# Kernel tuning notes

Measured on AMD Instinct MI355X. Metric: run time of the kernel, lower is better.

The kernel has to match this reference:

```python
import jax, jax.numpy as jnp
import numpy as np

FP8_MAX = 448.0  # max finite value of float8_e4m3fn


def _fp8_quant(v, scale):
    # emulate saturating scaled cast to float8_e4m3fn, then dequant-free fp8 storage (upcast to f32 for the gemm)
    q = jnp.clip(v / scale, -FP8_MAX, FP8_MAX)
    return q.astype(jnp.float8_e4m3fn).astype(jnp.float32)


def setup_inputs() -> dict:
    key = jax.random.key(0)
    k0, k1, k2, k3 = jax.random.split(key, 4)
    T, H, I, E = 1024, 1024, 2816, 8
    x = jax.random.normal(k0, (T, H), jnp.float32)
    router_logits = jax.random.normal(k1, (T, E), jnp.float32)
    w13_weight = jax.random.normal(k2, (E, 2 * I, H), jnp.float32) * 0.02
    w2_weight = jax.random.normal(k3, (E, H, I), jnp.float32) * 0.02
    return {
        "x": x,
        "router_logits": router_logits,
        "w13_weight": w13_weight,
        "w2_weight": w2_weight,
        "w13_input_scale": jnp.ones((E,), jnp.float32),
        "w2_input_scale": jnp.ones((E,), jnp.float32),
        "top_k": 2,
    }


def reference(x, router_logits, w13_weight, w2_weight, w13_input_scale, w2_input_scale, top_k):
    T, H = x.shape
    E, two_I, _ = w13_weight.shape
    I = two_I // 2

    # --- routing: softmax -> top_k -> renormalize (select_experts) ---
    probs = jax.nn.softmax(router_logits, axis=-1)
    topk_w, topk_ids = jax.lax.top_k(probs, top_k)            # [T,K]
    topk_w = topk_w / jnp.sum(topk_w, axis=-1, keepdims=True)
    # dense combine matrix [T,E]: sparsity of the grouped gemm dispatch
    combine = jnp.zeros((T, E), x.dtype).at[jnp.arange(T)[:, None], topk_ids].add(topk_w)

    # --- per-expert fp8 weight quantization (ops.scaled_fp8_quant per expert) ---
    w13_scale = jnp.max(jnp.abs(w13_weight), axis=(1, 2)) / FP8_MAX  # [E]
    w2_scale = jnp.max(jnp.abs(w2_weight), axis=(1, 2)) / FP8_MAX
    w13_q = _fp8_quant(w13_weight, w13_scale[:, None, None])         # [E,2I,H]
    w2_q = _fp8_quant(w2_weight, w2_scale[:, None, None])            # [E,H,I]

    # --- grouped gemm 1: per-expert activation quant + fp8 gemm + dequant scale ---
    x_q = _fp8_quant(x[None], w13_input_scale[:, None, None])        # [E,T,H]
    h = jnp.einsum('eth,eih->eti', x_q, w13_q) * (w13_input_scale * w13_scale)[:, None, None]

    # --- silu_and_mul: gate = first intermediate_size rows, up = second ---
    act = jax.nn.silu(h[..., :I]) * h[..., I:]                       # [E,T,I]

    # --- grouped gemm 2 ---
    act_q = _fp8_quant(act, w2_input_scale[:, None, None])
    o = jnp.einsum('eti,ehi->eth', act_q, w2_q) * (w2_input_scale * w2_scale)[:, None, None]

    # --- post_reorder: weighted combine of selected experts ---
    return jnp.einsum('te,eth->th', combine, o)                      # [T,H]
```

## Files before the change

kernel.cpp:

```cpp
#include <hip/hip_runtime.h>
#include <cstdint>
#include <cstddef>

#define T_TOK 1024
#define H_DIM 1024
#define I_DIM 2816
#define E_NUM 8
#define PAIRS 2048
#define KSPLIT 4
#define NT1 88
#define AMX2_X 32

typedef __attribute__((ext_vector_type(4))) float f32x4;
typedef __attribute__((ext_vector_type(4))) unsigned int u32x4;
typedef long i64;

__device__ __forceinline__ unsigned char fp8e4m3_sw(float v) {
  v = fminf(448.f, fmaxf(-448.f, v));
  unsigned b = __float_as_uint(v);
  unsigned s = (b >> 24) & 0x80u;
  float a = fabsf(v);
  if (a < 0.015625f) {
    int m = (int)rintf(a * 512.f);
    return (unsigned char)(s | (unsigned)m);
  }
  unsigned ab = b & 0x7fffffffu;
  unsigned rnd = 0x7FFFFu + ((ab >> 20) & 1u);
  ab += rnd;
  int e = (int)(ab >> 23) - 127;
  unsigned m = (ab >> 20) & 7u;
  if (e > 8 || (e == 8 && m > 6)) { e = 8; m = 6; }
  return (unsigned char)(s | (unsigned)((e + 7) << 3) | m);
}

__device__ __forceinline__ unsigned q4(float a, float b, float c, float d) {
#if __has_builtin(__builtin_amdgcn_cvt_pk_fp8_f32)
  unsigned w = (unsigned)__builtin_amdgcn_cvt_pk_fp8_f32(a, b, 0, false);
  return (unsigned)__builtin_amdgcn_cvt_pk_fp8_f32(c, d, (int)w, true);
#else
  return (unsigned)fp8e4m3_sw(a) | ((unsigned)fp8e4m3_sw(b) << 8) |
         ((unsigned)fp8e4m3_sw(c) << 16) | ((unsigned)fp8e4m3_sw(d) << 24);
#endif
}

__device__ __forceinline__ unsigned char q1(float a) {
#if __has_builtin(__builtin_amdgcn_cvt_pk_fp8_f32)
  return (unsigned char)((unsigned)__builtin_amdgcn_cvt_pk_fp8_f32(a, a, 0, false) & 0xFFu);
#else
  return fp8e4m3_sw(a);
#endif
}

__device__ __forceinline__ unsigned q4v(float4 f, float inv) {
  return q4(f.x * inv, f.y * inv, f.z * inv, f.w * inv);
}

__device__ __forceinline__ unsigned q4c(float4 f, float inv) {
  float a = fminf(448.f, fmaxf(-448.f, f.x * inv));
  float b = fminf(448.f, fmaxf(-448.f, f.y * inv));
  float c = fminf(448.f, fmaxf(-448.f, f.z * inv));
  float d = fminf(448.f, fmaxf(-448.f, f.w * inv));
  return q4(a, b, c, d);
}

__device__ __forceinline__ float wave_max(float m) {
#pragma unroll
  for (int off = 32; off > 0; off >>= 1) m = fmaxf(m, __shfl_xor(m, off));
  return m;
}

__device__ __forceinline__ void top2(const float* l, int& i0, int& i1) {
  i0 = 0; float b0 = l[0];
#pragma unroll
  for (int k = 1; k < E_NUM; k++) { if (l[k] > b0) { b0 = l[k]; i0 = k; } }
  i1 = -1; float b1 = -3.4e38f;
#pragma unroll
  for (int k = 0; k < E_NUM; k++) { if (k != i0 && l[k] > b1) { b1 = l[k]; i1 = k; } }
}

__global__ __launch_bounds__(256) void pre_k(const float* __restrict__ w13,
                                             const float* __restrict__ logits,
                                             const float* __restrict__ x,
                                             const float* __restrict__ s13,
                                             float* __restrict__ part13,
                                             int* __restrict__ cnt_g,
                                             int* __restrict__ offs_g,
                                             int* __restrict__ pair_xrow,
                                             float* __restrict__ pair_w,
                                             int* __restrict__ pairidx,
                                             unsigned char* __restrict__ Xq) {
  const int tid = threadIdx.x;
  if (blockIdx.x < 1024) {
    const int e = blockIdx.x >> 7, sub = blockIdx.x & 127;
    const float4* src = (const float4*)w13 + (size_t)e * (2 * I_DIM * H_DIM / 4);
    int idx = sub * 256 + tid;
    const int stride = 128 * 256;
    float m = 0.f;
#pragma unroll
    for (int j = 0; j < 44; j += 4) {
      float4 v0 = src[idx + (size_t)(j + 0) * stride];
      float4 v1 = src[idx + (size_t)(j + 1) * stride];
      float4 v2 = src[idx + (size_t)(j + 2) * stride];
      float4 v3 = src[idx + (size_t)(j + 3) * stride];
      m = fmaxf(m, fmaxf(fmaxf(fabsf(v0.x), fabsf(v0.y)), fmaxf(fabsf(v0.z), fabsf(v0.w))));
      m = fmaxf(m, fmaxf(fmaxf(fabsf(v1.x), fabsf(v1.y)), fmaxf(fabsf(v1.z), fabsf(v1.w))));
      m = fmaxf(m, fmaxf(fmaxf(fabsf(v2.x), fabsf(v2.y)), fmaxf(fabsf(v2.z), fabsf(v2.w))));
      m = fmaxf(m, fmaxf(fmaxf(fabsf(v3.x), fabsf(v3.y)), fmaxf(fabsf(v3.z), fabsf(v3.w))));
    }
    m = wave_max(m);
    __shared__ float wmax[4];
    int lane = tid & 63, wid = tid >> 6;
    if (lane == 0) wmax[wid] = m;
    __syncthreads();
    if (tid == 0)
      part13[blockIdx.x] = fmaxf(fmaxf(wmax[0], wmax[1]), fmaxf(wmax[2], wmax[3]));
    return;
  }

  if (blockIdx.x == 1024) {
    __shared__ int cnt_s[E_NUM], pos_s[E_NUM];
    if (tid < E_NUM) cnt_s[tid] = 0;
    __syncthreads();
    int i0s[4], i1s[4];
    float w0s[4], w1s[4];
#pragma unroll
    for (int j = 0; j < 4; j++) {
      int t = tid * 4 + j;
      float l[E_NUM];
#pragma unroll
      for (int k = 0; k < E_NUM; k++) l[k] = logits[t * E_NUM + k];
      int i0, i1;
      top2(l, i0, i1);
      float e1 = expf(l[i1] - l[i0]);
      float d = 1.f + e1;
      i0s[j] = i0; i1s[j] = i1; w0s[j] = 1.f / d; w1s[j] = e1 / d;
      atomicAdd(&cnt_s[i0], 1);
      atomicAdd(&cnt_s[i1], 1);
    }
    __syncthreads();
    if (tid == 0) {
      int s = 0;
#pragma unroll
      for (int e = 0; e < E_NUM; e++) {
        cnt_g[e] = cnt_s[e];
        offs_g[e] = s;
        pos_s[e] = s;
        s += cnt_s[e];
      }
      offs_g[E_NUM] = s;
    }
    __syncthreads();
#pragma unroll
    for (int j = 0; j < 4; j++) {
      int t = tid * 4 + j;
      int s0 = atomicAdd(&pos_s[i0s[j]], 1);
      pair_xrow[s0] = 2 * t; pair_w[s0] = w0s[j]; pairidx[2 * t] = s0;
      int s1 = atomicAdd(&pos_s[i1s[j]], 1);
      pair_xrow[s1] = 2 * t + 1; pair_w[s1] = w1s[j]; pairidx[2 * t + 1] = s1;
    }
    return;
  }

  {
    const int q = blockIdx.x - 1025;
#pragma unroll
    for (int j = 0; j < 2; j++) {
      int t = q * 2 + j;
      float l[E_NUM];
#pragma unroll
      for (int k = 0; k < E_NUM; k++) l[k] = logits[t * E_NUM + k];
      int i0, i1;
      top2(l, i0, i1);
      float inv0 = 1.f / s13[i0];
      float inv1 = 1.f / s13[i1];
      float4 v = ((const float4*)(x + (size_t)t * H_DIM))[tid];
      ((unsigned*)(Xq + (size_t)(2 * t) * H_DIM))[tid] = q4c(v, inv0);
      ((unsigned*)(Xq + (size_t)(2 * t + 1) * H_DIM))[tid] = q4c(v, inv1);
    }
  }
}

__global__ __launch_bounds__(512) void gemm1_k(const float* __restrict__ w13,
                                               const float* __restrict__ w2,
                                               const unsigned char* __restrict__ Xq,
                                               unsigned char* __restrict__ H1,
                                               const int* __restrict__ cnt,
                                               const int* __restrict__ offs,
                                               const float* __restrict__ part13,
                                               float* __restrict__ part2,
                                               const int* __restrict__ pair_xrow,
                                               const float* __restrict__ s13,
                                               const float* __restrict__ s2in) {
  const int e = blockIdx.z;
  const int tid = threadIdx.x, lane = tid & 63, wq = tid >> 6;

  if (blockIdx.x >= NT1) {
    const int bx2 = (blockIdx.x - NT1) * 4 + blockIdx.y;
    const float4* src = (const float4*)w2 + (size_t)e * (H_DIM * I_DIM / 4);
    int idx = bx2 * 512 + tid;
    const int stride = 128 * 512;
    float m = 0.f;
#pragma unroll
    for (int j = 0; j < 11; j++) {
      float4 v = src[idx + (size_t)j * stride];
      m = fmaxf(m, fmaxf(fmaxf(fabsf(v.x), fabsf(v.y)), fmaxf(fabsf(v.z), fabsf(v.w))));
    }
    m = wave_max(m);
    __shared__ float wmax2[8];
    if (lane == 0) wmax2[wq] = m;
    __syncthreads();
    if (tid == 0) {
      float mm = wmax2[0];
#pragma unroll
      for (int j = 1; j < 8; j++) mm = fmaxf(mm, wmax2[j]);
      part2[e * 128 + bx2] = mm;
    }
    return;
  }

  __shared__ float redA[8];
  {
    float v = part13[e * 128 + (tid & 127)];
    v = wave_max(v);
    if (lane == 0) redA[wq] = v;
  }
  __syncthreads();
  float amax = redA[0];
#pragma unroll
  for (int j = 1; j < 8; j++) amax = fmaxf(amax, redA[j]);

  const int count = cnt[e];
  const int m0 = blockIdx.y * 256;
  if (m0 >= count) return;
  const int nt = blockIdx.x;
  const int base = offs[e];

  const float inv_w = 448.f / amax;
  const float gs = s13[e] * (amax / 448.f);
  const float inv_a2 = 1.f / s2in[e];

  __shared__ __align__(16) unsigned char As[256][80];
  __shared__ __align__(16) unsigned char Bs[64][80];

  const int fr = lane & 15, ks = lane >> 4;

  f32x4 accg[2][2], accu[2][2];
#pragma unroll
  for (int i = 0; i < 2; i++)
#pragma unroll
    for (int j = 0; j < 2; j++) { accg[i][j] = (f32x4)0.f; accu[i][j] = (f32x4)0.f; }

  const int ar0 = tid >> 2, aseg = tid & 3;
  int pr0 = base + m0 + ar0;       if (pr0 > PAIRS - 1) pr0 = PAIRS - 1;
  int pr1 = base + m0 + ar0 + 128; if (pr1 > PAIRS - 1) pr1 = PAIRS - 1;
  const unsigned char* a_src0 = Xq + (size_t)pair_xrow[pr0] * H_DIM + aseg * 16;
  const unsigned char* a_src1 = Xq + (size_t)pair_xrow[pr1] * H_DIM + aseg * 16;

  const int brow = tid >> 3, bseg = tid & 7;
  const size_t brg = (size_t)nt * 32 + (brow & 31) + (size_t)(brow >> 5) * I_DIM;
  const float* b_src = w13 + ((size_t)e * 2 * I_DIM + brg) * H_DIM + bseg * 8;

  u32x4 ra0 = *(const u32x4*)a_src0;
  u32x4 ra1 = *(const u32x4*)a_src1;
  float4 fb0 = ((const float4*)b_src)[0], fb1 = ((const float4*)b_src)[1];
  unsigned qb0 = q4v(fb0, inv_w), qb1 = q4v(fb1, inv_w);

  for (int t = 0; t < H_DIM / 64; ++t) {
    __syncthreads();
    *(u32x4*)&As[ar0][aseg * 16] = ra0;
    *(u32x4*)&As[ar0 + 128][aseg * 16] = ra1;
    ((unsigned*)&Bs[brow][bseg * 8])[0] = qb0;
    ((unsigned*)&Bs[brow][bseg * 8])[1] = qb1;
    __syncthreads();
    if (t + 1 < H_DIM / 64) {
      int k0 = (t + 1) * 64;
      ra0 = *(const u32x4*)(a_src0 + k0);
      ra1 = *(const u32x4*)(a_src1 + k0);
      fb0 = ((const float4*)(b_src + k0))[0];
      fb1 = ((const float4*)(b_src + k0))[1];
    }
#pragma unroll
    for (int kk = 0; kk < 2; kk++) {
      i64 a0 = *(const i64*)&As[wq * 32 + fr][kk * 32 + ks * 8];
      i64 a1 = *(const i64*)&As[wq * 32 + 16 + fr][kk * 32 + ks * 8];
#pragma unroll
      for (int ni = 0; ni < 2; ni++) {
        i64 bg = *(const i64*)&Bs[ni * 16 + fr][kk * 32 + ks * 8];
        i64 bu = *(const i64*)&Bs[32 + ni * 16 + fr][kk * 32 + ks * 8];
        accg[0][ni] = __builtin_amdgcn_mfma_f32_16x16x32_fp8_fp8(a0, bg, accg[0][ni], 0, 0, 0);
        accg[1][ni] = __builtin_amdgcn_mfma_f32_16x16x32_fp8_fp8(a1, bg, accg[1][ni], 0, 0, 0);
        accu[0][ni] = __builtin_amdgcn_mfma_f32_16x16x32_fp8_fp8(a0, bu, accu[0][ni], 0, 0, 0);
        accu[1][ni] = __builtin_amdgcn_mfma_f32_16x16x32_fp8_fp8(a1, bu, accu[1][ni], 0, 0, 0);
      }
    }
    qb0 = q4v(fb0, inv_w);
    qb1 = q4v(fb1, inv_w);
  }

  const int rg = lane >> 4;
#pragma unroll
  for (int mi = 0; mi < 2; mi++) {
#pragma unroll
    for (int rr = 0; rr < 4; rr++) {
      int lrow = wq * 32 + mi * 16 + rg * 4 + rr;
      if (m0 + lrow < count) {
        size_t p = (size_t)(base + m0 + lrow);
#pragma unroll
        for (int ni = 0; ni < 2; ni++) {
          int col = nt * 32 + ni * 16 + fr;
          float g = accg[mi][ni][rr] * gs;
          float u = accu[mi][ni][rr] * gs;
          float act = g / (1.f + expf(-g)) * u * inv_a2;
          act = fminf(448.f, fmaxf(-448.f, act));
          H1[p * I_DIM + col] = q1(act);
        }
      }
    }
  }
}

__global__ __launch_bounds__(512) void gemm2_k(const float* __restrict__ w2,
                                               const unsigned char* __restrict__ H1,
                                               float* __restrict__ Op,
                                               const int* __restrict__ cnt,
                                               const int* __restrict__ offs,
                                               const float* __restrict__ part2,
                                               const float* __restrict__ s2in,
                                               const float* __restrict__ pair_w) {
  const int e = blockIdx.z;
  const int tid = threadIdx.x, lane = tid & 63, wq = tid >> 6;

  __shared__ float redA[8];
  {
    float v = part2[e * 128 + (tid & 127)];
    v = wave_max(v);
    if (lane == 0) redA[wq] = v;
  }
  __syncthreads();
  float amax = redA[0];
#pragma unroll
  for (int j = 1; j < 8; j++) amax = fmaxf(amax, redA[j]);

  const int count = cnt[e];
  const int m0 = blockIdx.y * 128;
  if (m0 >= count) return;
  const int nt = blockIdx.x & 15;
  const int ksp = blockIdx.x >> 4;
  const int n0 = nt * 64;
  const int base = offs[e];

  const float inv_w = 448.f / amax;
  const float s2 = s2in[e] * (amax / 448.f);

  __shared__ __align__(16) unsigned char As[128][80];
  __shared__ __align__(16) unsigned char Bs[64][80];

  const int fr = lane & 15, ks = lane >> 4;

  f32x4 acc[4];
#pragma unroll
  for (int i = 0; i < 4; i++) acc[i] = (f32x4)0.f;

  const int arow = tid >> 2, aseg = tid & 3;
  int pr = base + m0 + arow; if (pr > PAIRS - 1) pr = PAIRS - 1;
  const unsigned char* a_src = H1 + (size_t)pr * I_DIM + aseg * 16;

  const int brow = tid >> 3, bseg = tid & 7;
  const float* b_src = w2 + ((size_t)e * H_DIM + n0 + brow) * I_DIM + bseg * 8;

  const int KITER = (I_DIM / 64) / KSPLIT;
  const int kbase = ksp * KITER * 64;

  u32x4 ra = *(const u32x4*)(a_src + kbase);
  float4 fb0 = ((const float4*)(b_src + kbase))[0];
  float4 fb1 = ((const float4*)(b_src + kbase))[1];
  unsigned qb0 = q4v(fb0, inv_w), qb1 = q4v(fb1, inv_w);

  for (int t = 0; t < KITER; ++t) {
    __syncthreads();
    *(u32x4*)&As[arow][aseg * 16] = ra;
    ((unsigned*)&Bs[brow][bseg * 8])[0] = qb0;
    ((unsigned*)&Bs[brow][bseg * 8])[1] = qb1;
    __syncthreads();
    if (t + 1 < KITER) {
      int k0 = kbase + (t + 1) * 64;
      ra = *(const u32x4*)(a_src + k0);
      fb0 = ((const float4*)(b_src + k0))[0];
      fb1 = ((const float4*)(b_src + k0))[1];
    }
#pragma unroll
    for (int kk = 0; kk < 2; kk++) {
      i64 a0 = *(const i64*)&As[wq * 16 + fr][kk * 32 + ks * 8];
#pragma unroll
      for (int ni = 0; ni < 4; ni++) {
        i64 b = *(const i64*)&Bs[ni * 16 + fr][kk * 32 + ks * 8];
        acc[ni] = __builtin_amdgcn_mfma_f32_16x16x32_fp8_fp8(a0, b, acc[ni], 0, 0, 0);
      }
    }
    qb0 = q4v(fb0, inv_w);
    qb1 = q4v(fb1, inv_w);
  }

  const int rg = lane >> 4;
#pragma unroll
  for (int rr = 0; rr < 4; rr++) {
    int lrow = wq * 16 + rg * 4 + rr;
    if (m0 + lrow < count) {
      size_t p = (size_t)(base + m0 + lrow);
      float pw = pair_w[p];
#pragma unroll
      for (int ni = 0; ni < 4; ni++) {
        int col = n0 + ni * 16 + fr;
        Op[((size_t)ksp * PAIRS + p) * H_DIM + col] = acc[ni][rr] * s2 * pw;
      }
    }
  }
}

__global__ __launch_bounds__(256) void combine_k(const float* __restrict__ Op,
                                                 const int* __restrict__ pairidx,
                                                 float* __restrict__ out) {
  int t = blockIdx.x;
  int p0 = pairidx[2 * t], p1 = pairidx[2 * t + 1];
  f32x4 acc = (f32x4)0.f;
#pragma unroll
  for (int s = 0; s < KSPLIT; s++) {
    f32x4 a = ((const f32x4*)(Op + ((size_t)s * PAIRS + p0) * H_DIM))[threadIdx.x];
    f32x4 b = ((const f32x4*)(Op + ((size_t)s * PAIRS + p1) * H_DIM))[threadIdx.x];
    acc += a + b;
  }
  ((f32x4*)(out + (size_t)t * H_DIM))[threadIdx.x] = acc;
}

extern "C" void kernel_launch(void* const* d_in, const int* in_sizes, int n_in,
                              void* d_out, int out_size, void* d_ws, size_t ws_size,
                              hipStream_t stream) {
  (void)in_sizes; (void)n_in; (void)out_size; (void)ws_size;
  const float* x      = (const float*)d_in[0];
  const float* logits = (const float*)d_in[1];
  const float* w13    = (const float*)d_in[2];
  const float* w2     = (const float*)d_in[3];
  const float* s13    = (const float*)d_in[4];
  const float* s2in   = (const float*)d_in[5];
  float* out = (float*)d_out;

  char* ws = (char*)d_ws;
  int* cnt       = (int*)(ws + 128);
  int* offs      = (int*)(ws + 192);
  float* part13  = (float*)(ws + 4096);
  float* part2   = (float*)(ws + 8192);
  int* pair_xrow = (int*)(ws + 17408);
  float* pair_w  = (float*)(ws + 25600);
  int* pairidx   = (int*)(ws + 33792);
  unsigned char* Xq = (unsigned char*)(ws + (size_t)(1 << 20));
  unsigned char* H1 = (unsigned char*)(ws + (size_t)4 * (1 << 20));
  float* Op         = (float*)(ws + (size_t)10 * (1 << 20));

  pre_k<<<1537, 256, 0, stream>>>(w13, logits, x, s13, part13, cnt, offs,
                                  pair_xrow, pair_w, pairidx, Xq);

  gemm1_k<<<dim3(NT1 + AMX2_X, 4, E_NUM), 512, 0, stream>>>(
      w13, w2, Xq, H1, cnt, offs, part13, part2, pair_xrow, s13, s2in);

  gemm2_k<<<dim3(16 * KSPLIT, 8, E_NUM), 512, 0, stream>>>(
      w2, H1, Op, cnt, offs, part2, s2in, pair_w);

  combine_k<<<T_TOK, 256, 0, stream>>>(Op, pairidx, out);
}
```

Before: 164.8 us.

## Double-buffer shared-memory tiles in both grouped GEMM kernels

Both grouped GEMM kernels now use two LDS buffers for the A and B tiles. Each iteration writes the next tile into the alternate buffer while MFMAs consume the current one, and global loads are prefetched two tiles ahead. This cuts the per-iteration barrier count from two to one, aiming to overlap LDS stores and global latency with compute. The cost is double the shared memory per block, which may lower occupancy.

```diff
diff --git a/kernel.cpp b/kernel.cpp
--- a/kernel.cpp
+++ b/kernel.cpp
@@ -239,8 +239,8 @@
   const float gs = s13[e] * (amax / 448.f);
   const float inv_a2 = 1.f / s2in[e];
 
-  __shared__ __align__(16) unsigned char As[256][80];
-  __shared__ __align__(16) unsigned char Bs[64][80];
+  __shared__ __align__(16) unsigned char As[2][256][80];
+  __shared__ __align__(16) unsigned char Bs[2][64][80];
 
   const int fr = lane & 15, ks = lane >> 4;
 
@@ -260,20 +260,35 @@
   const size_t brg = (size_t)nt * 32 + (brow & 31) + (size_t)(brow >> 5) * I_DIM;
   const float* b_src = w13 + ((size_t)e * 2 * I_DIM + brg) * H_DIM + bseg * 8;
 
+  const int NIT = H_DIM / 64;
+
   u32x4 ra0 = *(const u32x4*)a_src0;
   u32x4 ra1 = *(const u32x4*)a_src1;
   float4 fb0 = ((const float4*)b_src)[0], fb1 = ((const float4*)b_src)[1];
+  {
+    unsigned q0 = q4v(fb0, inv_w), q1_ = q4v(fb1, inv_w);
+    *(u32x4*)&As[0][ar0][aseg * 16] = ra0;
+    *(u32x4*)&As[0][ar0 + 128][aseg * 16] = ra1;
+    ((unsigned*)&Bs[0][brow][bseg * 8])[0] = q0;
+    ((unsigned*)&Bs[0][brow][bseg * 8])[1] = q1_;
+  }
+  ra0 = *(const u32x4*)(a_src0 + 64);
+  ra1 = *(const u32x4*)(a_src1 + 64);
+  fb0 = ((const float4*)(b_src + 64))[0];
+  fb1 = ((const float4*)(b_src + 64))[1];
   unsigned qb0 = q4v(fb0, inv_w), qb1 = q4v(fb1, inv_w);
-
-  for (int t = 0; t < H_DIM / 64; ++t) {
-    __syncthreads();
-    *(u32x4*)&As[ar0][aseg * 16] = ra0;
-    *(u32x4*)&As[ar0 + 128][aseg * 16] = ra1;
-    ((unsigned*)&Bs[brow][bseg * 8])[0] = qb0;
-    ((unsigned*)&Bs[brow][bseg * 8])[1] = qb1;
-    __syncthreads();
-    if (t + 1 < H_DIM / 64) {
-      int k0 = (t + 1) * 64;
+  __syncthreads();
+
+  int c = 0;
+  for (int t = 0; t < NIT; ++t) {
+    if (t + 1 < NIT) {
+      *(u32x4*)&As[c ^ 1][ar0][aseg * 16] = ra0;
+      *(u32x4*)&As[c ^ 1][ar0 + 128][aseg * 16] = ra1;
+      ((unsigned*)&Bs[c ^ 1][brow][bseg * 8])[0] = qb0;
+      ((unsigned*)&Bs[c ^ 1][brow][bseg * 8])[1] = qb1;
+    }
+    if (t + 2 < NIT) {
+      int k0 = (t + 2) * 64;
       ra0 = *(const u32x4*)(a_src0 + k0);
       ra1 = *(const u32x4*)(a_src1 + k0);
       fb0 = ((const float4*)(b_src + k0))[0];
@@ -281,20 +296,24 @@
     }
 #pragma unroll
     for (int kk = 0; kk < 2; kk++) {
-      i64 a0 = *(const i64*)&As[wq * 32 + fr][kk * 32 + ks * 8];
-      i64 a1 = *(const i64*)&As[wq * 32 + 16 + fr][kk * 32 + ks * 8];
+      i64 a0 = *(const i64*)&As[c][wq * 32 + fr][kk * 32 + ks * 8];
+      i64 a1 = *(const i64*)&As[c][wq * 32 + 16 + fr][kk * 32 + ks * 8];
 #pragma unroll
       for (int ni = 0; ni < 2; ni++) {
-        i64 bg = *(const i64*)&Bs[ni * 16 + fr][kk * 32 + ks * 8];
-        i64 bu = *(const i64*)&Bs[32 + ni * 16 + fr][kk * 32 + ks * 8];
+        i64 bg = *(const i64*)&Bs[c][ni * 16 + fr][kk * 32 + ks * 8];
+        i64 bu = *(const i64*)&Bs[c][32 + ni * 16 + fr][kk * 32 + ks * 8];
         accg[0][ni] = __builtin_amdgcn_mfma_f32_16x16x32_fp8_fp8(a0, bg, accg[0][ni], 0, 0, 0);
         accg[1][ni] = __builtin_amdgcn_mfma_f32_16x16x32_fp8_fp8(a1, bg, accg[1][ni], 0, 0, 0);
         accu[0][ni] = __builtin_amdgcn_mfma_f32_16x16x32_fp8_fp8(a0, bu, accu[0][ni], 0, 0, 0);
         accu[1][ni] = __builtin_amdgcn_mfma_f32_16x16x32_fp8_fp8(a1, bu, accu[1][ni], 0, 0, 0);
       }
     }
-    qb0 = q4v(fb0, inv_w);
-    qb1 = q4v(fb1, inv_w);
+    if (t + 2 < NIT) {
+      qb0 = q4v(fb0, inv_w);
+      qb1 = q4v(fb1, inv_w);
+    }
+    __syncthreads();
+    c ^= 1;
   }
 
   const int rg = lane >> 4;
@@ -352,8 +371,8 @@
   const float inv_w = 448.f / amax;
   const float s2 = s2in[e] * (amax / 448.f);
 
-  __shared__ __align__(16) unsigned char As[128][80];
-  __shared__ __align__(16) unsigned char Bs[64][80];
+  __shared__ __align__(16) unsigned char As[2][128][80];
+  __shared__ __align__(16) unsigned char Bs[2][64][80];
 
   const int fr = lane & 15, ks = lane >> 4;
 
@@ -374,31 +393,46 @@
   u32x4 ra = *(const u32x4*)(a_src + kbase);
   float4 fb0 = ((const float4*)(b_src + kbase))[0];
   float4 fb1 = ((const float4*)(b_src + kbase))[1];
+  {
+    unsigned q0 = q4v(fb0, inv_w), q1_ = q4v(fb1, inv_w);
+    *(u32x4*)&As[0][arow][aseg * 16] = ra;
+    ((unsigned*)&Bs[0][brow][bseg * 8])[0] = q0;
+    ((unsigned*)&Bs[0][brow][bseg * 8])[1] = q1_;
+  }
+  ra = *(const u32x4*)(a_src + kbase + 64);
+  fb0 = ((const float4*)(b_src + kbase + 64))[0];
+  fb1 = ((const float4*)(b_src + kbase + 64))[1];
   unsigned qb0 = q4v(fb0, inv_w), qb1 = q4v(fb1, inv_w);
-
+  __syncthreads();
+
+  int c = 0;
   for (int t = 0; t < KITER; ++t) {
-    __syncthreads();
-    *(u32x4*)&As[arow][aseg * 16] = ra;
-    ((unsigned*)&Bs[brow][bseg * 8])[0] = qb0;
-    ((unsigned*)&Bs[brow][bseg * 8])[1] = qb1;
-    __syncthreads();
     if (t + 1 < KITER) {
-      int k0 = kbase + (t + 1) * 64;
+      *(u32x4*)&As[c ^ 1][arow][aseg * 16] = ra;
+      ((unsigned*)&Bs[c ^ 1][brow][bseg * 8])[0] = qb0;
+      ((unsigned*)&Bs[c ^ 1][brow][bseg * 8])[1] = qb1;
+    }
+    if (t + 2 < KITER) {
+      int k0 = kbase + (t + 2) * 64;
       ra = *(const u32x4*)(a_src + k0);
       fb0 = ((const float4*)(b_src + k0))[0];
       fb1 = ((const float4*)(b_src + k0))[1];
     }
 #pragma unroll
     for (int kk = 0; kk < 2; kk++) {
-      i64 a0 = *(const i64*)&As[wq * 16 + fr][kk * 32 + ks * 8];
+      i64 a0 = *(const i64*)&As[c][wq * 16 + fr][kk * 32 + ks * 8];
 #pragma unroll
       for (int ni = 0; ni < 4; ni++) {
-        i64 b = *(const i64*)&Bs[ni * 16 + fr][kk * 32 + ks * 8];
+        i64 b = *(const i64*)&Bs[c][ni * 16 + fr][kk * 32 + ks * 8];
         acc[ni] = __builtin_amdgcn_mfma_f32_16x16x32_fp8_fp8(a0, b, acc[ni], 0, 0, 0);
       }
     }
-    qb0 = q4v(fb0, inv_w);
-    qb1 = q4v(fb1, inv_w);
+    if (t + 2 < KITER) {
+      qb0 = q4v(fb0, inv_w);
+      qb1 = q4v(fb1, inv_w);
+    }
+    __syncthreads();
+    c ^= 1;
   }
 
   const int rg = lane >> 4;
```

After: 163.7 us (median of 2 runs). No clear change (-0.7%).
